# Performance work log

Measured on AMD Instinct MI355X. Metric: run time of the kernel, lower is better.

Reference implementation:

```python
import jax, jax.numpy as jnp
import numpy as np

INPUT_SIZE = 512
HIDDEN_SIZE = 2048
OUTPUT_SIZE = 512
NUM_LAYERS = 4
INNER = INPUT_SIZE + HIDDEN_SIZE  # 2560
BATCH = 4096


def setup_inputs() -> dict:
    key = jax.random.key(0)
    ks = jax.random.split(key, 5)
    scale = 1.0 / np.sqrt(INNER)  # kaiming-uniform-like scale for nn.Linear
    x = jax.random.normal(ks[0], (BATCH, INPUT_SIZE), dtype=jnp.float32)
    h = jax.random.normal(ks[1], (BATCH, HIDDEN_SIZE), dtype=jnp.float32)
    W_layers = jax.random.normal(ks[2], (NUM_LAYERS, INNER, INNER), dtype=jnp.float32) * scale
    b_layers = jnp.zeros((NUM_LAYERS, INNER), dtype=jnp.float32)
    W_i2h = jax.random.normal(ks[3], (HIDDEN_SIZE, INNER), dtype=jnp.float32) * scale
    b_i2h = jnp.zeros((HIDDEN_SIZE,), dtype=jnp.float32)
    W_i2o = jax.random.normal(ks[4], (OUTPUT_SIZE, INNER), dtype=jnp.float32) * scale
    b_i2o = jnp.zeros((OUTPUT_SIZE,), dtype=jnp.float32)
    return {"x": x, "h": h, "W_layers": W_layers, "b_layers": b_layers,
            "W_i2h": W_i2h, "b_i2h": b_i2h, "W_i2o": W_i2o, "b_i2o": b_i2o}


def reference(x, h, W_layers, b_layers, W_i2h, b_i2h, W_i2o, b_i2o):
    # combined: [B, inner]
    combined = jnp.concatenate([x, h], axis=1)
    # stack of square Hebbian linear layers + ReLU (imprint trace writes are
    # state side effects only; they do not affect the forward output)
    for l in range(W_layers.shape[0]):
        combined = jax.nn.relu(jnp.einsum('bi,oi->bo', combined, W_layers[l]) + b_layers[l])
    hidden = jnp.tanh(jnp.einsum('bi,oi->bo', combined, W_i2h) + b_i2h)
    output = jnp.einsum('bi,oi->bo', combined, W_i2o) + b_i2o
    return (output, hidden)
```

## Files before the change

kernel.cpp:

```cpp
#include <hip/hip_runtime.h>
#include <hip/hip_bf16.h>

#define BATCH 4096
#define IN_SZ 512
#define HID_SZ 2048
#define OUT_SZ 512
#define NLAYER 4
#define INNER 2560
#define NKT (INNER / 64)


typedef __attribute__((ext_vector_type(8))) short bf16x8;
typedef __attribute__((ext_vector_type(4))) float f32x4;

__device__ __forceinline__ unsigned short f2bf(float f) {
  unsigned int u = __float_as_uint(f);
  u += 0x7fff + ((u >> 16) & 1);
  return (unsigned short)(u >> 16);
}

__device__ __forceinline__ void gload16(const void* g, void* l) {
  __builtin_amdgcn_global_load_lds(
      (const __attribute__((address_space(1))) unsigned int*)g,
      (__attribute__((address_space(3))) unsigned int*)l,
      16, 0, 0);
}


#define NWL4  6553600
#define NWO4  327680
#define NWH4  1310720
__global__ void cvt_all(const float* __restrict__ Wl, const float* __restrict__ Wih,
                        const float* __restrict__ Wio, unsigned short* __restrict__ dst) {
  const int n4 = NWL4 + NWO4 + NWH4;
  int i = blockIdx.x * blockDim.x + threadIdx.x;
  const int stride = gridDim.x * blockDim.x;
  for (; i < n4; i += stride) {
    const float* src;
    long off4;
    if (i < NWL4) { src = Wl; off4 = i; }
    else if (i < NWL4 + NWO4) { src = Wio; off4 = i - NWL4; }
    else { src = Wih; off4 = i - NWL4 - NWO4; }
    float4 v = *reinterpret_cast<const float4*>(src + off4 * 4);
    ushort4 o;
    o.x = f2bf(v.x); o.y = f2bf(v.y); o.z = f2bf(v.z); o.w = f2bf(v.w);
    *reinterpret_cast<ushort4*>(dst + (long)i * 4) = o;
  }
}

__global__ void build_combined(const float* __restrict__ x,
                               const float* __restrict__ h,
                               unsigned short* __restrict__ out) {
  const int n4 = BATCH * INNER / 4;
  int i = blockIdx.x * blockDim.x + threadIdx.x;
  const int stride = gridDim.x * blockDim.x;
  for (; i < n4; i += stride) {
    int row = i / (INNER / 4);
    int c4 = i - row * (INNER / 4);
    const float* src = (c4 < IN_SZ / 4) ? (x + (long)row * IN_SZ + c4 * 4)
                                        : (h + (long)row * HID_SZ + (c4 - IN_SZ / 4) * 4);
    float4 v = *reinterpret_cast<const float4*>(src);
    ushort4 o;
    o.x = f2bf(v.x); o.y = f2bf(v.y); o.z = f2bf(v.z); o.w = f2bf(v.w);
    *reinterpret_cast<ushort4*>(out + (long)i * 4) = o;
  }
}


#define STAGE_U(kt, u, buf) do {                                              \
  if ((u) < 4) {                                                              \
    const int base_ = (u) * 32 + w * 8;                                       \
    gload16(A + (long)(row0 + base_ + srow) * INNER + (kt) * 64 + srcsw,      \
            (void*)(&lds[buf][base_ * 64]));                                  \
  } else {                                                                    \
    const int base_ = ((u) - 4) * 32 + w * 8;                                 \
    gload16(B + (long)(col0 + base_ + srow) * INNER + (kt) * 64 + srcsw,      \
            (void*)(&lds[buf][8192 + base_ * 64]));                           \
  } } while (0)

#define LOAD_AF(dst, mh, buf) do {                                           \
  const unsigned short* Ar_ = &lds[buf][0];                                  \
  _Pragma("unroll")                                                          \
  for (int m_ = 0; m_ < 2; ++m_) {                                           \
    int r_ = wr * 64 + (mh) * 32 + m_ * 16 + fr;                             \
    dst[m_][0] = *(const bf16x8*)(Ar_ + r_ * 64 + csw0);                     \
    dst[m_][1] = *(const bf16x8*)(Ar_ + r_ * 64 + csw1);                     \
  } } while (0)

#define LOAD_BQA(dst, buf) do {                                              \
  const unsigned short* Br_ = &lds[buf][8192];                               \
  _Pragma("unroll")                                                          \
  for (int n_ = 0; n_ < 3; ++n_) {                                           \
    int r_ = wcn * 80 + n_ * 16 + fr;                                        \
    dst[n_][0] = *(const bf16x8*)(Br_ + r_ * 64 + csw0);                     \
    dst[n_][1] = *(const bf16x8*)(Br_ + r_ * 64 + csw1);                     \
  } } while (0)

#define LOAD_BQB(dst, buf) do {                                              \
  const unsigned short* Br_ = &lds[buf][8192];                               \
  _Pragma("unroll")                                                          \
  for (int n_ = 0; n_ < 2; ++n_) {                                           \
    int r_ = wcn * 80 + (3 + n_) * 16 + fr;                                  \
    dst[n_][0] = *(const bf16x8*)(Br_ + r_ * 64 + csw0);                     \
    dst[n_][1] = *(const bf16x8*)(Br_ + r_ * 64 + csw1);                     \
  } } while (0)

#define MF_A(af, bq, mh) do {                                                 \
  __builtin_amdgcn_s_setprio(1);                                              \
  _Pragma("unroll")                                                           \
  for (int m_ = 0; m_ < 2; ++m_)                                              \
    _Pragma("unroll")                                                         \
    for (int n_ = 0; n_ < 3; ++n_) {                                          \
      acc[(mh) * 2 + m_][n_] = __builtin_amdgcn_mfma_f32_16x16x32_bf16(       \
          af[m_][0], bq[n_][0], acc[(mh) * 2 + m_][n_], 0, 0, 0);             \
      acc[(mh) * 2 + m_][n_] = __builtin_amdgcn_mfma_f32_16x16x32_bf16(       \
          af[m_][1], bq[n_][1], acc[(mh) * 2 + m_][n_], 0, 0, 0);             \
    }                                                                         \
  __builtin_amdgcn_s_setprio(0);                                              \
} while (0)

#define MF_B(af, bq, mh) do {                                                 \
  __builtin_amdgcn_s_setprio(1);                                              \
  _Pragma("unroll")                                                           \
  for (int m_ = 0; m_ < 2; ++m_)                                              \
    _Pragma("unroll")                                                         \
    for (int n_ = 0; n_ < 2; ++n_) {                                          \
      acc[(mh) * 2 + m_][3 + n_] = __builtin_amdgcn_mfma_f32_16x16x32_bf16(   \
          af[m_][0], bq[n_][0], acc[(mh) * 2 + m_][3 + n_], 0, 0, 0);         \
      acc[(mh) * 2 + m_][3 + n_] = __builtin_amdgcn_mfma_f32_16x16x32_bf16(   \
          af[m_][1], bq[n_][1], acc[(mh) * 2 + m_][3 + n_], 0, 0, 0);         \
    }                                                                         \
  __builtin_amdgcn_s_setprio(0);                                              \
} while (0)

#define SB() __builtin_amdgcn_sched_barrier(0)

#define TILE_BODY(d, AC, QC, AN, QN) do {                                     \
  const int T = T2 + (d);                                                     \
  const int kt1 = (T + 1 < NKT) ? T + 1 : NKT - 1;    \
  const int kt2 = (T + 2 < NKT) ? T + 2 : NKT - 1;                            \
        \
  LOAD_BQB(bqB, d);                                                           \
  STAGE_U(kt1, 6, (d) ^ 1); STAGE_U(kt1, 7, (d) ^ 1); STAGE_U(kt1, 8, (d) ^ 1); \
  SB();                                                                       \
  asm volatile("s_waitcnt lgkmcnt(4)" ::: "memory");          \
  SB();                                                                       \
  MF_A(AC, QC, 0);                                                            \
          \
  LOAD_AF(afB, 1, d);                                                         \
  STAGE_U(kt1, 0, (d) ^ 1); STAGE_U(kt1, 1, (d) ^ 1);                         \
  SB();                                                                       \
  asm volatile("s_waitcnt lgkmcnt(4)" ::: "memory");            \
  SB();                                                                       \
  MF_B(AC, bqB, 0);                                                           \
  __builtin_amdgcn_s_barrier();            \
           \
  STAGE_U(kt2, 4, d); STAGE_U(kt2, 5, d);                                     \
  SB();                                                                       \
  asm volatile("s_waitcnt lgkmcnt(0)" ::: "memory");            \
  SB();                                                                       \
  MF_B(afB, bqB, 1);                                                          \
  __builtin_amdgcn_s_barrier();                 \
       \
  STAGE_U(kt2, 2, d); STAGE_U(kt2, 3, d);                                     \
  asm volatile("s_waitcnt vmcnt(4)" ::: "memory");      \
  __builtin_amdgcn_s_barrier();            \
  SB();                                                                       \
  LOAD_AF(AN, 0, (d) ^ 1);                                                    \
  LOAD_BQA(QN, (d) ^ 1);                                                      \
  SB();                           \
  MF_A(afB, QC, 1);                                                           \
} while (0)

template <int MODE>
__global__ __launch_bounds__(256, 2)
void gemm8(const unsigned short* __restrict__ A, const unsigned short* __restrict__ B,
           const float* __restrict__ bias0, const float* __restrict__ bias1,
           void* __restrict__ C) {
  __shared__ unsigned short lds[2][18432];

  const int tid = threadIdx.x;
  const int w = tid >> 6;
  const int lane = tid & 63;

  const int flat = blockIdx.x;
  const int xcd = flat & 7;
  const int local = flat >> 3;
  const int nb = xcd * 2 + (local & 1);
  const int mb = local >> 1;
  const int row0 = mb * 128, col0 = nb * 160;
  const int wr = w >> 1, wcn = w & 1;

  const int srow = lane >> 3;
  const int srcsw = ((((lane & 7) << 4) ^ ((lane >> 3) << 4)) >> 1);

  const int fr = lane & 15;
  const int csw0 = ((((lane >> 4) << 4)) ^ ((lane & 7) << 4)) >> 1;
  const int csw1 = ((64 + ((lane >> 4) << 4)) ^ ((lane & 7) << 4)) >> 1;

  f32x4 acc[4][5] = {};
  bf16x8 afA0[2][2], afA1[2][2], afB[2][2];
  bf16x8 bqA0[3][2], bqA1[3][2], bqB[2][2];

  STAGE_U(0, 0, 0); STAGE_U(0, 1, 0); STAGE_U(0, 2, 0); STAGE_U(0, 3, 0);
  STAGE_U(0, 4, 0); STAGE_U(0, 5, 0); STAGE_U(0, 6, 0); STAGE_U(0, 7, 0);
  STAGE_U(0, 8, 0);
  STAGE_U(1, 4, 1); STAGE_U(1, 5, 1); STAGE_U(1, 2, 1); STAGE_U(1, 3, 1);
  asm volatile("s_waitcnt vmcnt(4)" ::: "memory");
  __builtin_amdgcn_s_barrier();
  SB();
  LOAD_AF(afA0, 0, 0);
  LOAD_BQA(bqA0, 0);
  SB();

  for (int T2 = 0; T2 < NKT; T2 += 2) {
    TILE_BODY(0, afA0, bqA0, afA1, bqA1);
    TILE_BODY(1, afA1, bqA1, afA0, bqA0);
  }
  asm volatile("s_waitcnt vmcnt(0) lgkmcnt(0)" ::: "memory");
  __builtin_amdgcn_s_barrier();

  if (MODE == 0) {
    unsigned short* eb = &lds[0][0];
#pragma unroll
    for (int n = 0; n < 5; ++n) {
      const int col = wcn * 80 + n * 16 + fr;
      const float bv = bias0[col0 + col];
#pragma unroll
      for (int m = 0; m < 4; ++m) {
        const int rbase = wr * 64 + m * 16 + ((lane >> 4) << 2);
#pragma unroll
        for (int j = 0; j < 4; ++j) {
          float v = fmaxf(acc[m][n][j] + bv, 0.0f);
          eb[(rbase + j) * 160 + col] = f2bf(v);
        }
      }
    }
    __builtin_amdgcn_s_barrier();
    unsigned short* Co = (unsigned short*)C;
#pragma unroll
    for (int r = 0; r < 10; ++r) {
      const int u = tid + r * 256;
      const int off = u * 8;
      const int row = off / 160;
      const int cole = off % 160;
      bf16x8 v = *reinterpret_cast<const bf16x8*>(eb + off);
      *reinterpret_cast<bf16x8*>(Co + (long)(row0 + row) * INNER + col0 + cole) = v;
    }
  } else {
    float* outO = (float*)C;
    float* outH = (float*)C + (long)BATCH * OUT_SZ;
    float* eb4 = (float*)&lds[0][0];
#pragma unroll
    for (int h2 = 0; h2 < 2; ++h2) {
      if (wr == h2) {
#pragma unroll
        for (int n = 0; n < 5; ++n) {
          const int col = wcn * 80 + n * 16 + fr;
          const int gc = col0 + col;
          const float bv = (gc < OUT_SZ) ? bias0[gc] : bias1[gc - OUT_SZ];
#pragma unroll
          for (int m = 0; m < 4; ++m) {
            const int rbase = m * 16 + ((lane >> 4) << 2);
#pragma unroll
            for (int j = 0; j < 4; ++j) {
              float v = acc[m][n][j] + bv;
              if (gc >= OUT_SZ) v = tanhf(v);
              eb4[(rbase + j) * 160 + col] = v;
            }
          }
        }
      }
      __builtin_amdgcn_s_barrier();
#pragma unroll
      for (int r = 0; r < 10; ++r) {
        const int u = tid + r * 256;
        const int off4 = u * 4;
        const int row = off4 / 160;
        const int cole = off4 % 160;
        const int gc = col0 + cole;
        float4 v = *reinterpret_cast<const float4*>(eb4 + off4);
        const int grow = row0 + h2 * 64 + row;
        if (gc < OUT_SZ)
          *reinterpret_cast<float4*>(outO + (long)grow * OUT_SZ + gc) = v;
        else
          *reinterpret_cast<float4*>(outH + (long)grow * HID_SZ + (gc - OUT_SZ)) = v;
      }
      __builtin_amdgcn_s_barrier();
    }
  }
}


extern "C" void kernel_launch(void* const* d_in, const int* in_sizes, int n_in,
                              void* d_out, int out_size, void* d_ws, size_t ws_size,
                              hipStream_t stream) {
  const float* x   = (const float*)d_in[0];
  const float* h   = (const float*)d_in[1];
  const float* Wl  = (const float*)d_in[2];
  const float* bl  = (const float*)d_in[3];
  const float* Wih = (const float*)d_in[4];
  const float* bih = (const float*)d_in[5];
  const float* Wio = (const float*)d_in[6];
  const float* bio = (const float*)d_in[7];

  unsigned short* ws   = (unsigned short*)d_ws;
  unsigned short* Wlb  = ws;
  unsigned short* Whb  = Wlb + (long)NLAYER * INNER * INNER;
  unsigned short* act0 = Whb + (long)INNER * INNER;
  unsigned short* act1 = act0 + (long)BATCH * INNER;

  cvt_all<<<2048, 256, 0, stream>>>(Wl, Wih, Wio, Wlb);
  build_combined<<<2048, 256, 0, stream>>>(x, h, act0);

  unsigned short* a_in = act0;
  unsigned short* a_out = act1;
  for (int l = 0; l < NLAYER; ++l) {
    gemm8<0><<<512, 256, 0, stream>>>(a_in, Wlb + (long)l * INNER * INNER,
                                      bl + (long)l * INNER, nullptr, a_out);
    unsigned short* t = a_in; a_in = a_out; a_out = t;
  }

  gemm8<1><<<512, 256, 0, stream>>>(a_in, Whb, bio, bih, d_out);
}
```

Before: 306.9 us.

## Overlap next-layer weight conversion with current GEMM via extra blocks

```diff
diff --git a/kernel.cpp b/kernel.cpp
--- a/kernel.cpp
+++ b/kernel.cpp
@@ -8,6 +8,7 @@
 #define NLAYER 4
 #define INNER 2560
 #define NKT (INNER / 64)
+#define NCVT 96
 
 
 typedef __attribute__((ext_vector_type(8))) short bf16x8;
@@ -26,43 +27,32 @@
       16, 0, 0);
 }
 
-
-#define NWL4  6553600
-#define NWO4  327680
-#define NWH4  1310720
-__global__ void cvt_all(const float* __restrict__ Wl, const float* __restrict__ Wih,
-                        const float* __restrict__ Wio, unsigned short* __restrict__ dst) {
-  const int n4 = NWL4 + NWO4 + NWH4;
+#define NW14 1638400
+#define NC4  2621440
+__global__ void prep(const float* __restrict__ W0, const float* __restrict__ x,
+                     const float* __restrict__ h, unsigned short* __restrict__ Wdst,
+                     unsigned short* __restrict__ cdst) {
+  const int total = NW14 + NC4;
   int i = blockIdx.x * blockDim.x + threadIdx.x;
   const int stride = gridDim.x * blockDim.x;
-  for (; i < n4; i += stride) {
+  for (; i < total; i += stride) {
     const float* src;
-    long off4;
-    if (i < NWL4) { src = Wl; off4 = i; }
-    else if (i < NWL4 + NWO4) { src = Wio; off4 = i - NWL4; }
-    else { src = Wih; off4 = i - NWL4 - NWO4; }
-    float4 v = *reinterpret_cast<const float4*>(src + off4 * 4);
-    ushort4 o;
-    o.x = f2bf(v.x); o.y = f2bf(v.y); o.z = f2bf(v.z); o.w = f2bf(v.w);
-    *reinterpret_cast<ushort4*>(dst + (long)i * 4) = o;
-  }
-}
-
-__global__ void build_combined(const float* __restrict__ x,
-                               const float* __restrict__ h,
-                               unsigned short* __restrict__ out) {
-  const int n4 = BATCH * INNER / 4;
-  int i = blockIdx.x * blockDim.x + threadIdx.x;
-  const int stride = gridDim.x * blockDim.x;
-  for (; i < n4; i += stride) {
-    int row = i / (INNER / 4);
-    int c4 = i - row * (INNER / 4);
-    const float* src = (c4 < IN_SZ / 4) ? (x + (long)row * IN_SZ + c4 * 4)
-                                        : (h + (long)row * HID_SZ + (c4 - IN_SZ / 4) * 4);
+    unsigned short* dst;
+    if (i < NW14) {
+      src = W0 + (long)i * 4;
+      dst = Wdst + (long)i * 4;
+    } else {
+      const int j = i - NW14;
+      const int row = j / (INNER / 4);
+      const int c4 = j - row * (INNER / 4);
+      src = (c4 < IN_SZ / 4) ? (x + (long)row * IN_SZ + c4 * 4)
+                             : (h + (long)row * HID_SZ + (c4 - IN_SZ / 4) * 4);
+      dst = cdst + (long)j * 4;
+    }
     float4 v = *reinterpret_cast<const float4*>(src);
     ushort4 o;
     o.x = f2bf(v.x); o.y = f2bf(v.y); o.z = f2bf(v.z); o.w = f2bf(v.w);
-    *reinterpret_cast<ushort4*>(out + (long)i * 4) = o;
+    *reinterpret_cast<ushort4*>(dst) = o;
   }
 }
 
@@ -176,14 +166,34 @@
 __global__ __launch_bounds__(256, 2)
 void gemm8(const unsigned short* __restrict__ A, const unsigned short* __restrict__ B,
            const float* __restrict__ bias0, const float* __restrict__ bias1,
-           void* __restrict__ C) {
+           void* __restrict__ C,
+           const float* __restrict__ cvtA, const float* __restrict__ cvtB,
+           int csplit, unsigned short* __restrict__ cvtD, int cvtN4) {
   __shared__ unsigned short lds[2][18432];
 
   const int tid = threadIdx.x;
+  const int flat = blockIdx.x;
+
+  if (flat >= 512) {
+    long i = (long)(flat - 512) * 256 + tid;
+    const long stride = (long)NCVT * 256;
+    for (; i < cvtN4; i += stride) {
+      const long e = i * 4;
+      const int row = (int)(e / INNER);
+      const int col = (int)(e - (long)row * INNER);
+      const float* sp = (row < csplit) ? (cvtA + (long)row * INNER + col)
+                                       : (cvtB + (long)(row - csplit) * INNER + col);
+      float4 v = *reinterpret_cast<const float4*>(sp);
+      ushort4 o;
+      o.x = f2bf(v.x); o.y = f2bf(v.y); o.z = f2bf(v.z); o.w = f2bf(v.w);
+      *reinterpret_cast<ushort4*>(cvtD + e) = o;
+    }
+    return;
+  }
+
   const int w = tid >> 6;
   const int lane = tid & 63;
 
-  const int flat = blockIdx.x;
   const int xcd = flat & 7;
   const int local = flat >> 3;
   const int nb = xcd * 2 + (local & 1);
@@ -232,7 +242,7 @@
 #pragma unroll
         for (int j = 0; j < 4; ++j) {
           float v = fmaxf(acc[m][n][j] + bv, 0.0f);
-          eb[(rbase + j) * 160 + col] = f2bf(v);
+          eb[(rbase + j) * 168 + col] = f2bf(v);
         }
       }
     }
@@ -244,7 +254,7 @@
       const int off = u * 8;
       const int row = off / 160;
       const int cole = off % 160;
-      bf16x8 v = *reinterpret_cast<const bf16x8*>(eb + off);
+      bf16x8 v = *reinterpret_cast<const bf16x8*>(eb + row * 168 + cole);
       *reinterpret_cast<bf16x8*>(Co + (long)(row0 + row) * INNER + col0 + cole) = v;
     }
   } else {
@@ -266,7 +276,7 @@
             for (int j = 0; j < 4; ++j) {
               float v = acc[m][n][j] + bv;
               if (gc >= OUT_SZ) v = tanhf(v);
-              eb4[(rbase + j) * 160 + col] = v;
+              eb4[(rbase + j) * 164 + col] = v;
             }
           }
         }
@@ -279,7 +289,7 @@
         const int row = off4 / 160;
         const int cole = off4 % 160;
         const int gc = col0 + cole;
-        float4 v = *reinterpret_cast<const float4*>(eb4 + off4);
+        float4 v = *reinterpret_cast<const float4*>(eb4 + row * 164 + cole);
         const int grow = row0 + h2 * 64 + row;
         if (gc < OUT_SZ)
           *reinterpret_cast<float4*>(outO + (long)grow * OUT_SZ + gc) = v;
@@ -310,16 +320,26 @@
   unsigned short* act0 = Whb + (long)INNER * INNER;
   unsigned short* act1 = act0 + (long)BATCH * INNER;
 
-  cvt_all<<<2048, 256, 0, stream>>>(Wl, Wih, Wio, Wlb);
-  build_combined<<<2048, 256, 0, stream>>>(x, h, act0);
+  const long WSZ = (long)INNER * INNER;
+  const int BIG = 1 << 30;
+
+  prep<<<2048, 256, 0, stream>>>(Wl, x, h, Wlb, act0);
 
   unsigned short* a_in = act0;
   unsigned short* a_out = act1;
   for (int l = 0; l < NLAYER; ++l) {
-    gemm8<0><<<512, 256, 0, stream>>>(a_in, Wlb + (long)l * INNER * INNER,
-                                      bl + (long)l * INNER, nullptr, a_out);
+    const float* cA; const float* cB; int split; unsigned short* cD;
+    if (l < NLAYER - 1) {
+      cA = Wl + (l + 1) * WSZ; cB = cA; split = BIG; cD = Wlb + (l + 1) * WSZ;
+    } else {
+      cA = Wio; cB = Wih; split = OUT_SZ; cD = Whb;
+    }
+    gemm8<0><<<512 + NCVT, 256, 0, stream>>>(a_in, Wlb + (long)l * WSZ,
+                                             bl + (long)l * INNER, nullptr, a_out,
+                                             cA, cB, split, cD, NW14);
     unsigned short* t = a_in; a_in = a_out; a_out = t;
   }
 
-  gemm8<1><<<512, 256, 0, stream>>>(a_in, Whb, bio, bih, d_out);
-}
+  gemm8<1><<<512, 256, 0, stream>>>(a_in, Whb, bio, bih, d_out,
+                                    Wl, Wl, BIG, Wlb, 0);
+}
```

Result: slower. 379.0 us (+23.5%).
